# Kernel optimization log

Hardware: AMD Instinct MI355X
Metric: run time of the kernel (lower is better)

## Reference

```python
import jax, jax.numpy as jnp
import numpy as np
from jax import lax

D_MODEL = 1024
D_STATE = 16
D_CONV = 4
EXPAND = 2
D_INNER = EXPAND * D_MODEL          # 2048
DT_RANK = (D_MODEL + 15) // 16      # 64


def setup_inputs() -> dict:
    key = jax.random.key(0)
    ks = jax.random.split(key, 12)
    B, L = 2, 2048
    s = lambda *sh: 1.0 / np.sqrt(sh[-1])
    inp = {
        "x": jax.random.normal(ks[0], (B, L, D_MODEL), jnp.float32),
        "in_proj_w": jax.random.normal(ks[1], (2 * D_INNER, D_MODEL), jnp.float32) * s(0, D_MODEL),
        "conv_w": jax.random.normal(ks[2], (D_INNER, 1, D_CONV), jnp.float32) * s(0, D_CONV),
        "conv_b": jax.random.normal(ks[3], (D_INNER,), jnp.float32) * 0.01,
        "x_proj_w": jax.random.normal(ks[4], (DT_RANK + 2 * D_STATE, D_INNER), jnp.float32) * s(0, D_INNER),
        "dt_proj_w": jax.random.normal(ks[5], (D_INNER, DT_RANK), jnp.float32) * s(0, DT_RANK),
        "dt_proj_b": jax.random.normal(ks[6], (D_INNER,), jnp.float32) * 0.1 - 4.0,  # softplus(dt) small
        "A_log": jnp.log(jnp.broadcast_to(jnp.arange(1, D_STATE + 1, dtype=jnp.float32), (D_INNER, D_STATE))),
        "D": jnp.ones((D_INNER,), jnp.float32),
        "out_proj_w": jax.random.normal(ks[7], (D_MODEL, D_INNER), jnp.float32) * s(0, D_INNER),
        "ln_w": jnp.ones((D_MODEL,), jnp.float32),
        "ln_b": jnp.zeros((D_MODEL,), jnp.float32),
    }
    return inp


def _mamba(x, in_proj_w, conv_w, conv_b, x_proj_w, dt_proj_w, dt_proj_b, A_log, D, out_proj_w):
    B, L, _ = x.shape
    xz = jnp.einsum("bld,ed->ble", x, in_proj_w)          # [B,L,2*d_inner]
    xi, z = jnp.split(xz, 2, axis=-1)                       # each [B,L,d_inner]

    # causal depthwise conv1d over time
    xt = jnp.transpose(xi, (0, 2, 1))                       # [B,d_inner,L]
    xc = lax.conv_general_dilated(
        xt, conv_w, window_strides=(1,), padding=[(D_CONV - 1, 0)],
        dimension_numbers=("NCH", "OIH", "NCH"), feature_group_count=D_INNER)
    xc = jax.nn.silu(xc + conv_b[None, :, None])            # [B,d_inner,L]
    u = jnp.transpose(xc, (0, 2, 1))                        # [B,L,d_inner]

    x_dbl = jnp.einsum("bld,ed->ble", u, x_proj_w)          # [B,L,dt_rank+2N]
    dt, Bm, Cm = jnp.split(x_dbl, [DT_RANK, DT_RANK + D_STATE], axis=-1)
    delta = jax.nn.softplus(jnp.einsum("blr,dr->bld", dt, dt_proj_w) + dt_proj_b)  # [B,L,d_inner]

    A = -jnp.exp(A_log)                                     # [d_inner,N]

    def step(h, inputs):
        d_t, B_t, C_t, u_t = inputs                         # [B,d], [B,N], [B,N], [B,d]
        dA = jnp.exp(d_t[..., None] * A)                    # [B,d_inner,N]
        h = dA * h + (d_t * u_t)[..., None] * B_t[:, None, :]
        y_t = jnp.einsum("bdn,bn->bd", h, C_t)
        return h, y_t

    xs = (jnp.transpose(delta, (1, 0, 2)), jnp.transpose(Bm, (1, 0, 2)),
          jnp.transpose(Cm, (1, 0, 2)), jnp.transpose(u, (1, 0, 2)))
    h0 = jnp.zeros((B, D_INNER, D_STATE), x.dtype)
    _, ys = lax.scan(step, h0, xs)                          # ys [L,B,d_inner]
    y = jnp.transpose(ys, (1, 0, 2)) + u * D                # skip connection
    y = y * jax.nn.silu(z)                                  # gate
    return jnp.einsum("bld,ed->ble", y, out_proj_w)         # [B,L,d_model]


def reference(x, in_proj_w, conv_w, conv_b, x_proj_w, dt_proj_w, dt_proj_b,
              A_log, D, out_proj_w, ln_w, ln_b):
    residual = x
    y = _mamba(x, in_proj_w, conv_w, conv_b, x_proj_w, dt_proj_w, dt_proj_b,
               A_log, D, out_proj_w)
    # dropout is identity in eval; residual + LayerNorm
    h = y + residual
    mu = jnp.mean(h, axis=-1, keepdims=True)
    var = jnp.var(h, axis=-1, keepdims=True)
    return (h - mu) * lax.rsqrt(var + 1e-5) * ln_w + ln_b
```

## Files before the change

### kernel.cpp

```cpp
#include <hip/hip_runtime.h>

typedef unsigned short u16;
typedef __attribute__((ext_vector_type(8))) short bf8_t;
typedef __attribute__((ext_vector_type(4))) float f4_t;
typedef __attribute__((ext_vector_type(4))) unsigned short u16x4;
typedef __attribute__((ext_vector_type(8))) unsigned short u16x8;

__device__ __forceinline__ float b2f(u16 h) {
  union { unsigned u; float f; } v; v.u = ((unsigned)h) << 16; return v.f;
}
__device__ __forceinline__ u16 f2b(float f) {
  union { float f; unsigned u; } v; v.f = f;
  unsigned u = v.u;
  u += 0x7fffu + ((u >> 16) & 1u);
  return (u16)(u >> 16);
}

#define AS1C(p) ((const __attribute__((address_space(1))) void*)(p))
#define AS3(p)  ((__attribute__((address_space(3))) void*)(p))

__global__ __launch_bounds__(256)
void cvt_all(const float* __restrict__ x, const float* __restrict__ inW,
             const float* __restrict__ xprojW, const float* __restrict__ dtW,
             const float* __restrict__ outW,
             u16* __restrict__ xb, u16* __restrict__ inWb, u16* __restrict__ xpb,
             u16* __restrict__ dtWb, u16* __restrict__ outWb)
{
  int i = blockIdx.x * 256 + threadIdx.x;
  if (i >= 2703360) return;
  const float* s; u16* d; int off;
  if (i < 1048576)      { s = x;      d = xb;    off = i; }
  else if (i < 2097152) { s = inW;    d = inWb;  off = i - 1048576; }
  else if (i < 2146304) { s = xprojW; d = xpb;   off = i - 2097152; }
  else if (i < 2179072) { s = dtW;    d = dtWb;  off = i - 2146304; }
  else                  { s = outW;   d = outWb; off = i - 2179072; }
  f4_t v = *(const f4_t*)(s + (size_t)off * 4);
  u16x4 o;
#pragma unroll
  for (int j = 0; j < 4; ++j) o[j] = f2b(v[j]);
  *(u16x4*)(d + (size_t)off * 4) = o;
}

__device__ __forceinline__ void stage64(const u16* g, int ld, int row0, int rowmax,
                                        int k0, u16* lds, int wid, int lane) {
  int qg = (lane & 7) ^ ((lane >> 3) & 7);
#pragma unroll
  for (int c = 0; c < 4; ++c) {
    int chunk = wid * 4 + c;
    int r = row0 + chunk * 8 + (lane >> 3);
    if (r > rowmax) r = rowmax;
    const u16* gp = g + (size_t)r * ld + k0 + qg * 8;
    __builtin_amdgcn_global_load_lds(AS1C(gp), AS3(lds + chunk * 512), 16, 0, 0);
  }
}

template<int EPI>
__device__ __forceinline__ void gemm_body(const u16* __restrict__ A, int lda,
             const u16* __restrict__ Bt, int ldb,
             int Kblk, int Nact,
             u16* __restrict__ o16, float* __restrict__ of32,
             float* __restrict__ of32b, const float* __restrict__ biasf)
{
  __shared__ u16 lsA[128 * 64];
  __shared__ u16 lsB[128 * 64];
  const int tid = threadIdx.x;
  const int wid = tid >> 6, lane = tid & 63;
  const int wm = wid >> 1, wn = wid & 1;
  const int lrow = lane & 15;
  const int kq = lane >> 4;
  const int sw = lrow & 7;
  const int m0 = blockIdx.y * 128;
  const int n0 = (EPI == 1) ? 0 : blockIdx.x * 128;
  int kbase = 0;
  if (EPI == 1) kbase = blockIdx.x * Kblk;
  if (EPI == 3) kbase = blockIdx.z * Kblk;

  f4_t acc[4][4];
#pragma unroll
  for (int i = 0; i < 4; ++i)
#pragma unroll
    for (int j = 0; j < 4; ++j) acc[i][j] = {0.f, 0.f, 0.f, 0.f};

  for (int kt = kbase; kt < kbase + Kblk; kt += 64) {
    stage64(A,  lda, m0, 0x3fffffff, kt, lsA, wid, lane);
    stage64(Bt, ldb, n0, Nact - 1,   kt, lsB, wid, lane);
    __syncthreads();
#pragma unroll
    for (int h = 0; h < 2; ++h) {
      const int lk = ((h * 4 + kq) ^ sw) * 8;
      bf8_t af[4], bfr[4];
#pragma unroll
      for (int mi = 0; mi < 4; ++mi)
        af[mi] = *(const bf8_t*)&lsA[(wm * 64 + mi * 16 + lrow) * 64 + lk];
#pragma unroll
      for (int ni = 0; ni < 4; ++ni)
        bfr[ni] = *(const bf8_t*)&lsB[(wn * 64 + ni * 16 + lrow) * 64 + lk];
#pragma unroll
      for (int mi = 0; mi < 4; ++mi)
#pragma unroll
        for (int ni = 0; ni < 4; ++ni)
          acc[mi][ni] = __builtin_amdgcn_mfma_f32_16x16x32_bf16(af[mi], bfr[ni], acc[mi][ni], 0, 0, 0);
    }
    __syncthreads();
  }

  const int rq = (lane >> 4) * 4;
#pragma unroll
  for (int mi = 0; mi < 4; ++mi) {
#pragma unroll
    for (int ni = 0; ni < 4; ++ni) {
#pragma unroll
      for (int r = 0; r < 4; ++r) {
        int m = m0 + wm * 64 + mi * 16 + rq + r;
        int n = n0 + wn * 64 + ni * 16 + lrow;
        float v = acc[mi][ni][r];
        if (EPI == 0) {
          if (n < 2048) o16[(size_t)m * 2048 + n] = f2b(v);
          else          o16[(size_t)8388608 + (size_t)m * 2048 + (n - 2048)] = f2b(v);
        } else if (EPI == 1) {
          if (n < 96) of32[((size_t)blockIdx.x * 4096 + m) * 96 + n] = v;
        } else if (EPI == 2) {
          float t = v + biasf[n];
          float sp = (t > 20.f) ? t : log1pf(__expf(t));
          o16[(size_t)m * 2048 + n] = f2b(sp);
        } else {
          float* dst = blockIdx.z ? of32b : of32;
          dst[(size_t)m * 1024 + n] = v;
        }
      }
    }
  }
}

__global__ __launch_bounds__(256)
void gemm_in(const u16* A, int lda, const u16* Bt, int ldb, int Kblk, int Nact,
             u16* o16, float* of32, float* of32b, const float* biasf)
{ gemm_body<0>(A, lda, Bt, ldb, Kblk, Nact, o16, of32, of32b, biasf); }

__global__ __launch_bounds__(256)
void gemm_xp(const u16* A, int lda, const u16* Bt, int ldb, int Kblk, int Nact,
             u16* o16, float* of32, float* of32b, const float* biasf)
{ gemm_body<1>(A, lda, Bt, ldb, Kblk, Nact, o16, of32, of32b, biasf); }

__global__ __launch_bounds__(256)
void gemm_dt(const u16* A, int lda, const u16* Bt, int ldb, int Kblk, int Nact,
             u16* o16, float* of32, float* of32b, const float* biasf)
{ gemm_body<2>(A, lda, Bt, ldb, Kblk, Nact, o16, of32, of32b, biasf); }

__global__ __launch_bounds__(256)
void gemm_out(const u16* A, int lda, const u16* Bt, int ldb, int Kblk, int Nact,
              u16* o16, float* of32, float* of32b, const float* biasf)
{ gemm_body<3>(A, lda, Bt, ldb, Kblk, Nact, o16, of32, of32b, biasf); }

__global__ __launch_bounds__(256)
void xproj_reduce(const float* __restrict__ part, u16* __restrict__ dtA,
                  float* __restrict__ bc)
{
  int idx = blockIdx.x * 256 + threadIdx.x;
  int m = idx / 96, n = idx - m * 96;
  float s = 0.f;
#pragma unroll
  for (int p = 0; p < 8; ++p) s += part[(size_t)p * 393216 + idx];
  if (n < 64) dtA[(size_t)m * 64 + n] = f2b(s);
  else        bc[(size_t)m * 32 + (n - 64)] = s;
}

__global__ __launch_bounds__(256)
void conv_silu(const u16* __restrict__ xib, const float* __restrict__ cw,
               const float* __restrict__ cb, u16* __restrict__ ub)
{
  int i = blockIdx.x * 256 + threadIdx.x;
  int c8 = (i & 255) * 8;
  int row = i >> 8;
  int l = row & 2047;
  const u16* base = xib + (size_t)row * 2048 + c8;
  u16x8 x0 = {0,0,0,0,0,0,0,0}, x1 = x0, x2 = x0, x3;
  x3 = *(const u16x8*)(base);
  if (l >= 1) x2 = *(const u16x8*)(base - 2048);
  if (l >= 2) x1 = *(const u16x8*)(base - 2 * 2048);
  if (l >= 3) x0 = *(const u16x8*)(base - 3 * 2048);
  f4_t cb0 = *(const f4_t*)(cb + c8);
  f4_t cb1 = *(const f4_t*)(cb + c8 + 4);
  u16x8 o;
#pragma unroll
  for (int j = 0; j < 8; ++j) {
    f4_t w = *(const f4_t*)(cw + (size_t)(c8 + j) * 4);
    float a = (j < 4 ? cb0[j] : cb1[j - 4])
            + w[0] * b2f(x0[j]) + w[1] * b2f(x1[j])
            + w[2] * b2f(x2[j]) + w[3] * b2f(x3[j]);
    float s = a / (1.f + __expf(-a));
    o[j] = f2b(s);
  }
  *(u16x8*)(ub + (size_t)row * 2048 + c8) = o;
}

__global__ __launch_bounds__(256)
void scan_s1(const u16* __restrict__ delta_bf, const u16* __restrict__ ub,
             const float* __restrict__ bc, const float* __restrict__ alog,
             u16* __restrict__ S, float* __restrict__ Q)
{
  int blk = blockIdx.x;
  int g = blk & 7, c = (blk >> 3) & 63, b = blk >> 9;
  int d = g * 256 + threadIdx.x;
  float Av[16];
#pragma unroll
  for (int nq = 0; nq < 4; ++nq) {
    f4_t al = *(const f4_t*)(alog + (size_t)d * 16 + nq * 4);
#pragma unroll
    for (int j = 0; j < 4; ++j) Av[nq * 4 + j] = -__expf(al[j]);
  }
  float Av0 = Av[0];
  bool st = true;
#pragma unroll
  for (int n = 1; n < 16; ++n)
    st = st && (fabsf(Av[n] - (float)(n + 1) * Av0) <= 1e-3f * (float)(n + 1));
  f4_t Qr[4];
#pragma unroll
  for (int nq = 0; nq < 4; ++nq) Qr[nq] = {0.f,0.f,0.f,0.f};
  float Sd = 0.f;
  int row0 = b * 2048 + c * 32;
  if (st) {
#pragma unroll 2
    for (int i = 0; i < 32; ++i) {
      size_t row = (size_t)(row0 + i);
      float dlt = b2f(delta_bf[row * 2048 + d]);
      float uv  = b2f(ub[row * 2048 + d]);
      const float* bp = bc + row * 32;
      f4_t Bv[4];
#pragma unroll
      for (int nq = 0; nq < 4; ++nq) Bv[nq] = *(const f4_t*)(bp + nq * 4);
      float du = dlt * uv;
      float e1 = __expf(dlt * Av0);
      float a = e1;
      Sd += dlt;
#pragma unroll
      for (int n = 0; n < 16; ++n) {
        Qr[n >> 2][n & 3] = a * Qr[n >> 2][n & 3] + du * Bv[n >> 2][n & 3];
        a *= e1;
      }
    }
  } else {
#pragma unroll 2
    for (int i = 0; i < 32; ++i) {
      size_t row = (size_t)(row0 + i);
      float dlt = b2f(delta_bf[row * 2048 + d]);
      float uv  = b2f(ub[row * 2048 + d]);
      const float* bp = bc + row * 32;
      f4_t Bv[4];
#pragma unroll
      for (int nq = 0; nq < 4; ++nq) Bv[nq] = *(const f4_t*)(bp + nq * 4);
      float du = dlt * uv;
      Sd += dlt;
#pragma unroll
      for (int n = 0; n < 16; ++n) {
        float a = __expf(dlt * Av[n]);
        Qr[n >> 2][n & 3] = a * Qr[n >> 2][n & 3] + du * Bv[n >> 2][n & 3];
      }
    }
  }
  S[(size_t)(b * 64 + c) * 2048 + d] = f2b(Sd);
  size_t o = ((size_t)((b * 64 + c) * 2048 + d)) * 16;
#pragma unroll
  for (int nq = 0; nq < 4; ++nq)
    *(f4_t*)(Q + o + nq * 4) = Qr[nq];
}

__global__ __launch_bounds__(256)
void scan_comb(const u16* __restrict__ S16, float* __restrict__ Q,
               const float* __restrict__ alog)
{
  int idx = blockIdx.x * 256 + threadIdx.x;
  int b = idx >> 15, dn = idx & 32767;
  int d = dn >> 4;
  float Av = -__expf(alog[dn]);
  size_t qbase = (size_t)b * 2097152 + dn;
  size_t sbase = (size_t)b * 131072 + d;
  float H = 0.f;
#pragma unroll
  for (int cg = 0; cg < 4; ++cg) {
    float sv[16], qv[16];
#pragma unroll
    for (int j = 0; j < 16; ++j) {
      int c = cg * 16 + j;
      qv[j] = Q[qbase + (size_t)c * 32768];
      sv[j] = b2f(S16[sbase + (size_t)c * 2048]);
    }
#pragma unroll
    for (int j = 0; j < 16; ++j) {
      int c = cg * 16 + j;
      Q[qbase + (size_t)c * 32768] = H;
      H = __expf(Av * sv[j]) * H + qv[j];
    }
  }
}

__global__ __launch_bounds__(256)
void scan_s3(const u16* __restrict__ delta_bf, const u16* __restrict__ ub,
             const float* __restrict__ bc, const float* __restrict__ alog,
             const float* __restrict__ Q, const float* __restrict__ Dw,
             u16* __restrict__ zy)
{
  int blk = blockIdx.x;
  int g = blk & 7, c = (blk >> 3) & 63, b = blk >> 9;
  int d = g * 256 + threadIdx.x;
  float Av[16];
#pragma unroll
  for (int nq = 0; nq < 4; ++nq) {
    f4_t al = *(const f4_t*)(alog + (size_t)d * 16 + nq * 4);
#pragma unroll
    for (int j = 0; j < 4; ++j) Av[nq * 4 + j] = -__expf(al[j]);
  }
  float Av0 = Av[0];
  bool st = true;
#pragma unroll
  for (int n = 1; n < 16; ++n)
    st = st && (fabsf(Av[n] - (float)(n + 1) * Av0) <= 1e-3f * (float)(n + 1));
  f4_t h4[4];
  size_t o = ((size_t)((b * 64 + c) * 2048 + d)) * 16;
#pragma unroll
  for (int nq = 0; nq < 4; ++nq) h4[nq] = *(const f4_t*)(Q + o + nq * 4);
  float Dv = Dw[d];
  int row0 = b * 2048 + c * 32;
  if (st) {
#pragma unroll 2
    for (int i = 0; i < 32; ++i) {
      size_t row = (size_t)(row0 + i);
      float dlt = b2f(delta_bf[row * 2048 + d]);
      float uv  = b2f(ub[row * 2048 + d]);
      const float* bp = bc + row * 32;
      f4_t Bv[4], Cv[4];
#pragma unroll
      for (int nq = 0; nq < 4; ++nq) { Bv[nq] = *(const f4_t*)(bp + nq * 4); Cv[nq] = *(const f4_t*)(bp + 16 + nq * 4); }
      float du = dlt * uv;
      float e1 = __expf(dlt * Av0);
      float a = e1;
      float y = 0.f;
#pragma unroll
      for (int n = 0; n < 16; ++n) {
        float hn = a * h4[n >> 2][n & 3] + du * Bv[n >> 2][n & 3];
        h4[n >> 2][n & 3] = hn;
        y += hn * Cv[n >> 2][n & 3];
        a *= e1;
      }
      float zv = b2f(zy[row * 2048 + d]);
      float ov = (y + Dv * uv) * (zv / (1.f + __expf(-zv)));
      zy[row * 2048 + d] = f2b(ov);
    }
  } else {
#pragma unroll 2
    for (int i = 0; i < 32; ++i) {
      size_t row = (size_t)(row0 + i);
      float dlt = b2f(delta_bf[row * 2048 + d]);
      float uv  = b2f(ub[row * 2048 + d]);
      const float* bp = bc + row * 32;
      f4_t Bv[4], Cv[4];
#pragma unroll
      for (int nq = 0; nq < 4; ++nq) { Bv[nq] = *(const f4_t*)(bp + nq * 4); Cv[nq] = *(const f4_t*)(bp + 16 + nq * 4); }
      float du = dlt * uv;
      float y = 0.f;
#pragma unroll
      for (int n = 0; n < 16; ++n) {
        float a = __expf(dlt * Av[n]);
        float hn = a * h4[n >> 2][n & 3] + du * Bv[n >> 2][n & 3];
        h4[n >> 2][n & 3] = hn;
        y += hn * Cv[n >> 2][n & 3];
      }
      float zv = b2f(zy[row * 2048 + d]);
      float ov = (y + Dv * uv) * (zv / (1.f + __expf(-zv)));
      zy[row * 2048 + d] = f2b(ov);
    }
  }
}

__global__ __launch_bounds__(256)
void ln_kernel(const float* __restrict__ hp0, const float* __restrict__ hp1,
               const float* __restrict__ xin,
               const float* __restrict__ lnw, const float* __restrict__ lnb,
               float* __restrict__ outp)
{
  __shared__ float ssum[4], ssq[4];
  int row = blockIdx.x, t = threadIdx.x;
  f4_t h0 = *(const f4_t*)(hp0 + (size_t)row * 1024 + t * 4);
  f4_t h1 = *(const f4_t*)(hp1 + (size_t)row * 1024 + t * 4);
  f4_t xv = *(const f4_t*)(xin + (size_t)row * 1024 + t * 4);
  float v[4], s = 0.f, q = 0.f;
#pragma unroll
  for (int j = 0; j < 4; ++j) { v[j] = h0[j] + h1[j] + xv[j]; s += v[j]; q += v[j] * v[j]; }
#pragma unroll
  for (int m = 32; m; m >>= 1) { s += __shfl_xor(s, m, 64); q += __shfl_xor(q, m, 64); }
  int wv = t >> 6;
  if ((t & 63) == 0) { ssum[wv] = s; ssq[wv] = q; }
  __syncthreads();
  s = ssum[0] + ssum[1] + ssum[2] + ssum[3];
  q = ssq[0] + ssq[1] + ssq[2] + ssq[3];
  float mu = s * (1.f / 1024.f);
  float var = q * (1.f / 1024.f) - mu * mu;
  float rs = rsqrtf(var + 1e-5f);
  f4_t o;
#pragma unroll
  for (int j = 0; j < 4; ++j)
    o[j] = (v[j] - mu) * rs * lnw[t * 4 + j] + lnb[t * 4 + j];
  *(f4_t*)(outp + (size_t)row * 1024 + t * 4) = o;
}

extern "C" void kernel_launch(void* const* d_in, const int* in_sizes, int n_in,
                              void* d_out, int out_size, void* d_ws, size_t ws_size,
                              hipStream_t stream)
{
  const float* x      = (const float*)d_in[0];
  const float* inW    = (const float*)d_in[1];
  const float* convW  = (const float*)d_in[2];
  const float* convB  = (const float*)d_in[3];
  const float* xprojW = (const float*)d_in[4];
  const float* dtW    = (const float*)d_in[5];
  const float* dtB    = (const float*)d_in[6];
  const float* alog   = (const float*)d_in[7];
  const float* Dw     = (const float*)d_in[8];
  const float* outW   = (const float*)d_in[9];
  const float* lnw    = (const float*)d_in[10];
  const float* lnb    = (const float*)d_in[11];
  float* out = (float*)d_out;

  char* ws = (char*)d_ws;
  u16*   xiz    = (u16*)(ws);
  u16*   zy     = xiz + 8388608;
  u16*   xb     = (u16*)(ws + 33554432);
  u16*   inWb   = xb + 4194304;
  u16*   u_bf   = (u16*)(ws + 33554432);
  u16*   dtA    = (u16*)(ws + 50331648);
  float* bc     = (float*)(ws + 50855936);
  u16*   xprojWb= (u16*)(ws + 51380224);
  u16*   dtWb   = (u16*)(ws + 51773440);
  u16*   outWb  = (u16*)(ws + 52035584);
  u16*   delta  = xiz;
  float* hpart1 = (float*)(ws);
  float* hpart0 = (float*)d_out;
  float* xpart  = (float*)d_out;
  u16*   Sbuf   = dtA;
  float* Qbuf   = (float*)d_out;

  dim3 blk(256);
  cvt_all<<<10560, blk, 0, stream>>>(x, inW, xprojW, dtW, outW,
                                     xb, inWb, xprojWb, dtWb, outWb);
  gemm_in<<<dim3(32, 32), blk, 0, stream>>>(xb, 1024, inWb, 1024, 1024, 4096, xiz, nullptr, nullptr, nullptr);
  conv_silu<<<4096, blk, 0, stream>>>(xiz, convW, convB, u_bf);
  gemm_xp<<<dim3(8, 32), blk, 0, stream>>>(u_bf, 2048, xprojWb, 2048, 256, 96, nullptr, xpart, nullptr, nullptr);
  xproj_reduce<<<1536, blk, 0, stream>>>(xpart, dtA, bc);
  gemm_dt<<<dim3(16, 32), blk, 0, stream>>>(dtA, 64, dtWb, 64, 64, 2048, delta, nullptr, nullptr, dtB);
  scan_s1<<<1024, blk, 0, stream>>>(delta, u_bf, bc, alog, Sbuf, Qbuf);
  scan_comb<<<256, blk, 0, stream>>>(Sbuf, Qbuf, alog);
  scan_s3<<<1024, blk, 0, stream>>>(delta, u_bf, bc, alog, Qbuf, Dw, zy);
  gemm_out<<<dim3(8, 32, 2), blk, 0, stream>>>(zy, 2048, outWb, 2048, 1024, 1024, nullptr, hpart0, hpart1, nullptr);
  ln_kernel<<<4096, blk, 0, stream>>>(hpart0, hpart1, x, lnw, lnb, out);
}
```

Before: 320.9 us.

## Replace in_proj GEMM with 256x256-tile 8-wave double-buffered pipelined kernel

Replaces the generic 128x128-tile in_proj GEMM with a dedicated kernel that uses 256x256 tiles and 512 threads (8 waves, each computing 128x64). It double-buffers LDS through direct global-to-LDS loads and interleaves staging of the next K slice with the MFMA quarters, using explicit waitcnt, barriers and setprio. The aim is more operand reuse per loaded byte and global-load latency hidden behind matrix math. In exchange the grid shrinks to 256 blocks, and the hand-written wait counts and schedule are fragile.

```diff
diff --git a/kernel.cpp b/kernel.cpp
--- a/kernel.cpp
+++ b/kernel.cpp
@@ -114,10 +114,7 @@
         int m = m0 + wm * 64 + mi * 16 + rq + r;
         int n = n0 + wn * 64 + ni * 16 + lrow;
         float v = acc[mi][ni][r];
-        if (EPI == 0) {
-          if (n < 2048) o16[(size_t)m * 2048 + n] = f2b(v);
-          else          o16[(size_t)8388608 + (size_t)m * 2048 + (n - 2048)] = f2b(v);
-        } else if (EPI == 1) {
+        if (EPI == 1) {
           if (n < 96) of32[((size_t)blockIdx.x * 4096 + m) * 96 + n] = v;
         } else if (EPI == 2) {
           float t = v + biasf[n];
@@ -133,11 +130,6 @@
 }
 
 __global__ __launch_bounds__(256)
-void gemm_in(const u16* A, int lda, const u16* Bt, int ldb, int Kblk, int Nact,
-             u16* o16, float* of32, float* of32b, const float* biasf)
-{ gemm_body<0>(A, lda, Bt, ldb, Kblk, Nact, o16, of32, of32b, biasf); }
-
-__global__ __launch_bounds__(256)
 void gemm_xp(const u16* A, int lda, const u16* Bt, int ldb, int Kblk, int Nact,
              u16* o16, float* of32, float* of32b, const float* biasf)
 { gemm_body<1>(A, lda, Bt, ldb, Kblk, Nact, o16, of32, of32b, biasf); }
@@ -151,6 +143,156 @@
 void gemm_out(const u16* A, int lda, const u16* Bt, int ldb, int Kblk, int Nact,
               u16* o16, float* of32, float* of32b, const float* biasf)
 { gemm_body<3>(A, lda, Bt, ldb, Kblk, Nact, o16, of32, of32b, biasf); }
+
+
+__device__ __forceinline__ void stageu(const u16* __restrict__ g, int ld,
+                                       int row0, int k0, u16* ldsu,
+                                       int wid, int lane) {
+  int qg = (lane & 7) ^ ((lane >> 3) & 7);
+#pragma unroll
+  for (int j = 0; j < 2; ++j) {
+    int rr = j * 64 + wid * 8 + (lane >> 3);
+    const u16* gp = g + (size_t)(row0 + rr) * ld + k0 + qg * 8;
+    __builtin_amdgcn_global_load_lds(AS1C(gp), AS3(ldsu + (j * 512 + wid * 64) * 8), 16, 0, 0);
+  }
+}
+
+#define G8_BAR()   __builtin_amdgcn_s_barrier()
+#define G8_LGKM0() do { asm volatile("s_waitcnt lgkmcnt(0)" ::: "memory"); \
+                        __builtin_amdgcn_sched_barrier(0); } while (0)
+#define G8_LGKM8() asm volatile("s_waitcnt lgkmcnt(8)" ::: "memory")
+#define G8_VM(N)   do { asm volatile("s_waitcnt vmcnt(" #N ")" ::: "memory"); \
+                        __builtin_amdgcn_sched_barrier(0); } while (0)
+
+#define RD_A(base, MH) do { \
+  _Pragma("unroll") \
+  for (int mi_ = 0; mi_ < 4; ++mi_) { \
+    af[mi_][0] = *(const bf8_t*)((base) + arow + ((MH) * 64 + mi_ * 16) * 64 + aq0); \
+    af[mi_][1] = *(const bf8_t*)((base) + arow + ((MH) * 64 + mi_ * 16) * 64 + aq1); \
+  } } while (0)
+
+#define RD_B(base, NH) do { \
+  _Pragma("unroll") \
+  for (int ni_ = 0; ni_ < 2; ++ni_) { \
+    bfr[NH][ni_][0] = *(const bf8_t*)((base) + brow + ((NH) * 32 + ni_ * 16) * 64 + aq0); \
+    bfr[NH][ni_][1] = *(const bf8_t*)((base) + brow + ((NH) * 32 + ni_ * 16) * 64 + aq1); \
+  } } while (0)
+
+#define MMA(MH, NH) do { \
+  __builtin_amdgcn_s_setprio(1); \
+  _Pragma("unroll") \
+  for (int mi_ = 0; mi_ < 4; ++mi_) \
+    _Pragma("unroll") \
+    for (int ni_ = 0; ni_ < 2; ++ni_) { \
+      acc[(MH) * 4 + mi_][(NH) * 2 + ni_] = __builtin_amdgcn_mfma_f32_16x16x32_bf16( \
+          af[mi_][0], bfr[NH][ni_][0], acc[(MH) * 4 + mi_][(NH) * 2 + ni_], 0, 0, 0); \
+      acc[(MH) * 4 + mi_][(NH) * 2 + ni_] = __builtin_amdgcn_mfma_f32_16x16x32_bf16( \
+          af[mi_][1], bfr[NH][ni_][1], acc[(MH) * 4 + mi_][(NH) * 2 + ni_], 0, 0, 0); \
+    } \
+  __builtin_amdgcn_s_setprio(0); \
+} while (0)
+
+__global__ __launch_bounds__(512, 2)
+void gemm8_in(const u16* __restrict__ A, const u16* __restrict__ Bt,
+              u16* __restrict__ o16)
+{
+  __shared__ u16 ls[65536];
+  const int tid = threadIdx.x;
+  const int wid = tid >> 6, lane = tid & 63;
+  const int wm = wid >> 2, wn = wid & 3;
+  const int lrow = lane & 15;
+  const int kq = lane >> 4;
+  const int sw = lrow & 7;
+  const int m0 = blockIdx.y * 256;
+  const int n0 = blockIdx.x * 256;
+  u16* lsA0 = ls;
+  u16* lsB0 = ls + 16384;
+  u16* lsA1 = ls + 32768;
+  u16* lsB1 = ls + 49152;
+  const int arow = (wm * 128 + lrow) * 64;
+  const int brow = (wn * 64 + lrow) * 64;
+  const int aq0 = (kq ^ sw) * 8;
+  const int aq1 = ((4 + kq) ^ sw) * 8;
+
+  f4_t acc[8][4];
+#pragma unroll
+  for (int i = 0; i < 8; ++i)
+#pragma unroll
+    for (int j = 0; j < 4; ++j) acc[i][j] = {0.f, 0.f, 0.f, 0.f};
+  bf8_t af[4][2];
+  bf8_t bfr[2][2][2];
+
+  stageu(A,  1024, m0,        0, lsA0,        wid, lane);
+  stageu(A,  1024, m0 + 128,  0, lsA0 + 8192, wid, lane);
+  stageu(Bt, 1024, n0,        0, lsB0,        wid, lane);
+  stageu(Bt, 1024, n0 + 128,  0, lsB0 + 8192, wid, lane);
+  stageu(Bt, 1024, n0,       64, lsB1,        wid, lane);
+  stageu(Bt, 1024, n0 + 128, 64, lsB1 + 8192, wid, lane);
+  G8_VM(4); G8_BAR();
+
+#pragma unroll 1
+  for (int i = 0; i < 7; ++i) {
+    const int k1 = (2 * i + 1) * 64, k2 = k1 + 64, k3 = k1 + 128;
+    RD_A(lsA0, 0); RD_B(lsB0, 0);
+    stageu(A, 1024, m0, k1, lsA1, wid, lane);
+    G8_LGKM8(); G8_BAR(); G8_LGKM0(); MMA(0, 0); G8_BAR();
+    RD_B(lsB0, 1);
+    stageu(A, 1024, m0 + 128, k1, lsA1 + 8192, wid, lane);
+    G8_BAR(); G8_LGKM0(); MMA(0, 1); G8_BAR();
+    RD_A(lsA0, 1);
+    stageu(Bt, 1024, n0, k2, lsB0, wid, lane);
+    G8_BAR(); G8_LGKM0(); MMA(1, 0); G8_BAR();
+    stageu(Bt, 1024, n0 + 128, k2, lsB0 + 8192, wid, lane);
+    G8_BAR(); G8_LGKM0(); MMA(1, 1); G8_VM(4); G8_BAR();
+    RD_A(lsA1, 0); RD_B(lsB1, 0);
+    stageu(A, 1024, m0, k2, lsA0, wid, lane);
+    G8_LGKM8(); G8_BAR(); G8_LGKM0(); MMA(0, 0); G8_BAR();
+    RD_B(lsB1, 1);
+    stageu(A, 1024, m0 + 128, k2, lsA0 + 8192, wid, lane);
+    G8_BAR(); G8_LGKM0(); MMA(0, 1); G8_BAR();
+    RD_A(lsA1, 1);
+    stageu(Bt, 1024, n0, k3, lsB1, wid, lane);
+    G8_BAR(); G8_LGKM0(); MMA(1, 0); G8_BAR();
+    stageu(Bt, 1024, n0 + 128, k3, lsB1 + 8192, wid, lane);
+    G8_BAR(); G8_LGKM0(); MMA(1, 1); G8_VM(4); G8_BAR();
+  }
+
+  {
+    const int k1 = 960;
+    RD_A(lsA0, 0); RD_B(lsB0, 0);
+    stageu(A, 1024, m0, k1, lsA1, wid, lane);
+    G8_LGKM8(); G8_BAR(); G8_LGKM0(); MMA(0, 0); G8_BAR();
+    RD_B(lsB0, 1);
+    stageu(A, 1024, m0 + 128, k1, lsA1 + 8192, wid, lane);
+    G8_BAR(); G8_LGKM0(); MMA(0, 1); G8_BAR();
+    RD_A(lsA0, 1);
+    G8_BAR(); G8_LGKM0(); MMA(1, 0); G8_BAR();
+    G8_BAR(); G8_LGKM0(); MMA(1, 1); G8_VM(0); G8_BAR();
+    RD_A(lsA1, 0); RD_B(lsB1, 0);
+    G8_BAR(); G8_LGKM0(); MMA(0, 0); G8_BAR();
+    RD_B(lsB1, 1);
+    G8_BAR(); G8_LGKM0(); MMA(0, 1); G8_BAR();
+    RD_A(lsA1, 1);
+    G8_BAR(); G8_LGKM0(); MMA(1, 0); G8_BAR();
+    G8_LGKM0(); MMA(1, 1);
+  }
+
+  const int rq = (lane >> 4) * 4;
+#pragma unroll
+  for (int mi = 0; mi < 8; ++mi) {
+#pragma unroll
+    for (int ni = 0; ni < 4; ++ni) {
+#pragma unroll
+      for (int r = 0; r < 4; ++r) {
+        int m = m0 + wm * 128 + mi * 16 + rq + r;
+        int n = n0 + wn * 64 + ni * 16 + lrow;
+        float v = acc[mi][ni][r];
+        if (n < 2048) o16[(size_t)m * 2048 + n] = f2b(v);
+        else          o16[(size_t)8388608 + (size_t)m * 2048 + (n - 2048)] = f2b(v);
+      }
+    }
+  }
+}
 
 __global__ __launch_bounds__(256)
 void xproj_reduce(const float* __restrict__ part, u16* __restrict__ dtA,
@@ -442,7 +584,7 @@
   dim3 blk(256);
   cvt_all<<<10560, blk, 0, stream>>>(x, inW, xprojW, dtW, outW,
                                      xb, inWb, xprojWb, dtWb, outWb);
-  gemm_in<<<dim3(32, 32), blk, 0, stream>>>(xb, 1024, inWb, 1024, 1024, 4096, xiz, nullptr, nullptr, nullptr);
+  gemm8_in<<<dim3(16, 16), dim3(512), 0, stream>>>(xb, inWb, xiz);
   conv_silu<<<4096, blk, 0, stream>>>(xiz, convW, convB, u_bf);
   gemm_xp<<<dim3(8, 32), blk, 0, stream>>>(u_bf, 2048, xprojWb, 2048, 256, 96, nullptr, xpart, nullptr, nullptr);
   xproj_reduce<<<1536, blk, 0, stream>>>(xpart, dtA, bc);
```

After: 311.9 us. -2.8%, faster.
